# Kernel optimization log

Hardware: AMD Instinct MI355X
Metric: run time of the kernel (lower is better)

The kernel has to match this reference:

```python
import jax, jax.numpy as jnp
import numpy as np

B, S, T = 1024, 1024, 32
TAGS = ["O"] + [p + f"T{i}" for i in range(1, 16) for p in ("B-", "I-")] + ["B-T16"]
MASKED = -1.0e4


def _init_params(key):
    bound = float(np.sqrt(6.0 / T))
    k1, k2, k3 = jax.random.split(key, 3)
    start = np.array(jax.random.uniform(k1, (T,), minval=-bound, maxval=bound))
    trans = np.array(jax.random.uniform(k2, (T, T), minval=-bound, maxval=bound))
    end = np.array(jax.random.uniform(k3, (T,), minval=-bound, maxval=bound))
    # structural BIO masking, as in _initialize_parameters
    for i, src in enumerate(TAGS):
        if src.startswith("I-"):
            start[i] = MASKED
        for j, tgt in enumerate(TAGS):
            if (src.startswith("B-") or src.startswith("I-")) and tgt.startswith("I-") and src[2:] != tgt[2:]:
                trans[i, j] = MASKED
            elif src == "O" and tgt.startswith("I-"):
                trans[i, j] = MASKED
    return jnp.asarray(start, jnp.float32), jnp.asarray(trans, jnp.float32), jnp.asarray(end, jnp.float32)


def setup_inputs() -> dict:
    key = jax.random.key(0)
    k_em, k_tag, k_len, k_par = jax.random.split(key, 4)
    emissions = jax.random.normal(k_em, (B, S, T), dtype=jnp.float32)
    tags = jax.random.randint(k_tag, (B, S), 0, T, dtype=jnp.int64) if jax.config.jax_enable_x64 else jax.random.randint(k_tag, (B, S), 0, T).astype(jnp.int32)
    lengths = jax.random.randint(k_len, (B,), S // 4, S + 1)
    mask = jnp.arange(S)[None, :] < lengths[:, None]  # prefix mask, bool [B, S]
    start_transitions, transitions, end_transitions = _init_params(k_par)
    return {
        "emissions": emissions,
        "tags": tags,
        "mask": mask,
        "start_transitions": start_transitions,
        "transitions": transitions,
        "end_transitions": end_transitions,
    }


def reference(emissions, tags, mask, start_transitions, transitions, end_transitions):
    b, s, t = emissions.shape
    ar = jnp.arange(s)
    bidx = jnp.arange(b)
    head = jnp.min(jnp.where(mask, ar[None, :], s - 1), axis=1)  # [B]
    tail = jnp.max(ar[None, :] * mask, axis=1)                   # [B]
    nonempty = mask.sum(axis=1) != 0

    # condition[:, j-1] == (mask[:, j] and head != j), for j = 1..S-1
    cond = mask[:, 1:] & (head[:, None] != ar[None, 1:])  # [B, S-1]

    # ---- numerator (gold path score): additive, fully vectorized ----
    head_tags = tags[bidx, head]
    tail_tags = tags[bidx, tail]
    em_tag = jnp.take_along_axis(emissions, tags[:, :, None], axis=2)[:, :, 0]  # [B, S]
    trans_step = transitions[tags[:, :-1], tags[:, 1:]]                          # [B, S-1]
    numerator = (start_transitions[head_tags]
                 + em_tag[bidx, head]
                 + jnp.sum(jnp.where(cond, trans_step + em_tag[:, 1:], 0.0), axis=1)
                 + end_transitions[tail_tags])
    numerator = jnp.where(nonempty, numerator, 0.0)

    # ---- denominator (log partition): scan over time ----
    score0 = start_transitions[None, :] + emissions[bidx, head]  # [B, T]

    def step(score, xs):
        em_j, cond_j = xs  # [B, T], [B]
        nxt = jax.nn.logsumexp(score[:, :, None] + transitions[None, :, :] + em_j[:, None, :], axis=1)
        return jnp.where(cond_j[:, None], nxt, score), None

    em_seq = jnp.moveaxis(emissions[:, 1:, :], 1, 0)  # [S-1, B, T]
    cond_seq = jnp.moveaxis(cond, 1, 0)               # [S-1, B]
    score_final, _ = jax.lax.scan(step, score0, (em_seq, cond_seq))
    denominator = jax.nn.logsumexp(score_final + end_transitions[None, :], axis=1)
    denominator = jnp.where(nonempty, denominator, 0.0)

    # ---- token_mean reduction ----
    llh = denominator - numerator
    labels = mask.sum(axis=1).astype(emissions.dtype)
    eps = 1e-6
    return jnp.sum(llh / (labels + eps)) / (jnp.sum(labels != 0).astype(emissions.dtype) + eps)
```

## Files before the change

### kernel.cpp

```cpp
#include <hip/hip_runtime.h>
#include <cstdint>

static constexpr int S = 1024;
static constexpr int T = 32;
static constexpr float L2E  = 1.4426950408889634f;
static constexpr float LN2f = 0.6931471805599453f;

typedef __attribute__((ext_vector_type(8)))  short  short8;
typedef __attribute__((ext_vector_type(16))) float  float16;

union Frag { unsigned u[4]; short8 s; };

__global__ void crf_zero(float* ws) { ws[0] = 0.0f; ws[1] = 0.0f; }

__global__ void crf_fin(const float* __restrict__ ws, float* __restrict__ out) {
  out[0] = ws[0] / (ws[1] + 1e-6f);
}

__device__ __forceinline__ float bcast_lane(float v, int k) {
  return __uint_as_float((unsigned)__builtin_amdgcn_readlane((int)__float_as_uint(v), k));
}

__device__ __forceinline__ unsigned packbf(float hi, float lo) {
  unsigned h = __float_as_uint(hi), l = __float_as_uint(lo);
  return ((h + 0x8000u) & 0xFFFF0000u) | ((l + 0x8000u) >> 16);
}

__device__ __forceinline__ void plswap(unsigned& x, unsigned& y, bool hih) {
#if __has_builtin(__builtin_amdgcn_permlane32_swap)
  auto r = __builtin_amdgcn_permlane32_swap((int)x, (int)y, false, false);
  x = (unsigned)r[0]; y = (unsigned)r[1];
#else
  unsigned ex = (unsigned)__shfl_xor((int)x, 32, 64);
  unsigned ey = (unsigned)__shfl_xor((int)y, 32, 64);
  unsigned nx = hih ? ey : x;
  unsigned ny = hih ? y  : ex;
  x = nx; y = ny;
#endif
}

__global__ __launch_bounds__(512, 4) void crf_main(
    const float* __restrict__ em, const int* __restrict__ tags,
    const int* __restrict__ mask, const float* __restrict__ startT,
    const float* __restrict__ trans, const float* __restrict__ endT,
    float* __restrict__ ws)
{
  __shared__ __align__(16) float s_g[8][512];
  __shared__ __align__(16) float s_mats[8][1024];
  __shared__ float s_trans[1024];
  __shared__ int   s_tags[1024];
  __shared__ unsigned long long s_mb[16];
  __shared__ int   s_head, s_tail, s_cnt, s_K[8];
  __shared__ float s_num[8];

  const int tid = threadIdx.x;
  const int l   = tid & 63;
  const int wv  = tid >> 6;
  const int b   = blockIdx.x;
  const int n   = l & 31;
  const int h   = l >> 5;
  const bool hih = (h == 1);

  const float* emb   = em   + (size_t)b * S * T;
  const int*   maskb = mask + (size_t)b * S;
  const int*   tagsb = tags + (size_t)b * S;

  for (int i = tid; i < 1024; i += 512) { s_tags[i] = tagsb[i]; s_trans[i] = trans[i]; }
  {
    unsigned long long b0 = __ballot(maskb[wv * 128 + l] != 0);
    unsigned long long b1 = __ballot(maskb[wv * 128 + 64 + l] != 0);
    if (l == 0) { s_mb[2 * wv] = b0; s_mb[2 * wv + 1] = b1; }
  }

  Frag Alo, Ahi;
  #pragma unroll
  for (int p = 0; p < 4; ++p) {
    int k0 = 8 * h + 2 * p;
    Alo.u[p] = packbf(exp2f(trans[(k0 + 1)  * T + n] * L2E),
                      exp2f(trans[(k0 + 0)  * T + n] * L2E));
    Ahi.u[p] = packbf(exp2f(trans[(k0 + 17) * T + n] * L2E),
                      exp2f(trans[(k0 + 16) * T + n] * L2E));
  }
  __syncthreads();

  if (wv == 0) {
    int first = 0x7fffffff, last = -1, pc = 0;
    if (l < 16) {
      unsigned long long w = s_mb[l];
      if (w) {
        first = 64 * l + (int)__builtin_ctzll(w);
        last  = 64 * l + 63 - (int)__builtin_clzll(w);
        pc    = (int)__builtin_popcountll(w);
      }
    }
    #pragma unroll
    for (int d = 1; d < 64; d <<= 1) {
      first = min(first, __shfl_xor(first, d));
      last  = max(last,  __shfl_xor(last,  d));
      pc   += __shfl_xor(pc, d);
    }
    if (l == 0) { s_head = first; s_tail = last; s_cnt = pc; }
  }
  __syncthreads();
  const int cnt  = s_cnt;
  const int head = (cnt > 0) ? s_head : 0;
  const int tail = (cnt > 0) ? s_tail : 0;

  float* sgw = s_g[wv];
  Frag Blo, Bhi;
  #pragma unroll
  for (int p = 0; p < 4; ++p) {
    int k0 = 8 * h + 2 * p;
    Blo.u[p] = ((k0 == n)      ? 0x3F80u : 0u) | ((k0 + 1  == n) ? 0x3F800000u : 0u);
    Bhi.u[p] = ((k0 + 16 == n) ? 0x3F80u : 0u) | ((k0 + 17 == n) ? 0x3F800000u : 0u);
  }
  int   Kacc  = 0;
  float numer = 0.0f;
  const int cs = wv * 128;

#define FOLD(JJ, RSC) do {                                                   \
    const float* gr = sgw + (JJ) * T + 4 * h;                                \
    float4 ga = *(const float4*)(gr);                                        \
    float4 gb = *(const float4*)(gr + 8);                                    \
    float4 gc = *(const float4*)(gr + 16);                                   \
    float4 gd = *(const float4*)(gr + 24);                                   \
    float16 D = {0,0,0,0,0,0,0,0,0,0,0,0,0,0,0,0};                           \
    D = __builtin_amdgcn_mfma_f32_32x32x16_bf16(Alo.s, Blo.s, D, 0, 0, 0);   \
    D = __builtin_amdgcn_mfma_f32_32x32x16_bf16(Ahi.s, Bhi.s, D, 0, 0, 0);   \
    D[0]  *= ga.x; D[1]  *= ga.y; D[2]  *= ga.z; D[3]  *= ga.w;              \
    D[4]  *= gb.x; D[5]  *= gb.y; D[6]  *= gb.z; D[7]  *= gb.w;              \
    D[8]  *= gc.x; D[9]  *= gc.y; D[10] *= gc.z; D[11] *= gc.w;              \
    D[12] *= gd.x; D[13] *= gd.y; D[14] *= gd.z; D[15] *= gd.w;              \
    if (RSC) {                                                               \
      float mx = fmaxf(fmaxf(fmaxf(D[0], D[1]), fmaxf(D[2], D[3])),          \
                       fmaxf(fmaxf(D[4], D[5]), fmaxf(D[6], D[7])));         \
      mx = fmaxf(mx, fmaxf(fmaxf(fmaxf(D[8], D[9]),  fmaxf(D[10], D[11])),   \
                           fmaxf(fmaxf(D[12], D[13]), fmaxf(D[14], D[15]))));\
      mx = fmaxf(mx, __shfl_xor(mx, 1));  mx = fmaxf(mx, __shfl_xor(mx, 2)); \
      mx = fmaxf(mx, __shfl_xor(mx, 4));  mx = fmaxf(mx, __shfl_xor(mx, 8)); \
      mx = fmaxf(mx, __shfl_xor(mx, 16)); mx = fmaxf(mx, __shfl_xor(mx, 32));\
      int E = (int)((__float_as_uint(mx) >> 23) & 0xffu);                    \
      float sc = __uint_as_float((unsigned)(254 - E) << 23);                 \
      Kacc += E - 127;                                                       \
      _Pragma("unroll")                                                      \
      for (int q_ = 0; q_ < 16; ++q_) D[q_] *= sc;                           \
    }                                                                        \
    unsigned u0 = packbf(D[1],  D[0]),  u1 = packbf(D[3],  D[2]);            \
    unsigned u2 = packbf(D[5],  D[4]),  u3 = packbf(D[7],  D[6]);            \
    unsigned u4 = packbf(D[9],  D[8]),  u5 = packbf(D[11], D[10]);           \
    unsigned u6 = packbf(D[13], D[12]), u7 = packbf(D[15], D[14]);           \
    plswap(u0, u2, hih); plswap(u1, u3, hih);                                \
    plswap(u4, u6, hih); plswap(u5, u7, hih);                                \
    Blo.u[0] = u0; Blo.u[1] = u1; Blo.u[2] = u2; Blo.u[3] = u3;              \
    Bhi.u[0] = u4; Bhi.u[1] = u5; Bhi.u[2] = u6; Bhi.u[3] = u7;              \
  } while (0)

  for (int sb = 0; sb < 8; ++sb) {
    const int j0 = cs + 16 * sb;
    if (j0 > tail) break;
    unsigned eff = (unsigned)((s_mb[j0 >> 6] >> (j0 & 63)) & 0xFFFFull);
    if (j0 == 0) eff &= ~1u;
    if (head >= j0 && head < j0 + 16) eff &= ~(1u << (head - j0));
    if (eff == 0) continue;

    {
      const float4* src = (const float4*)(emb + (size_t)j0 * T);
      float4 v0 = src[l], v1 = src[l + 64];
      v0.x = exp2f(v0.x * L2E); v0.y = exp2f(v0.y * L2E);
      v0.z = exp2f(v0.z * L2E); v0.w = exp2f(v0.w * L2E);
      v1.x = exp2f(v1.x * L2E); v1.y = exp2f(v1.y * L2E);
      v1.z = exp2f(v1.z * L2E); v1.w = exp2f(v1.w * L2E);
      ((float4*)sgw)[l] = v0; ((float4*)sgw)[l + 64] = v1;
    }

    if (l < 16 && ((eff >> l) & 1u)) {
      int j  = j0 + l;
      int tg = s_tags[j], tp = s_tags[j - 1];
      numer += s_trans[tp * T + tg] + log2f(sgw[l * T + tg]) * LN2f;
    }

    if (eff == 0xFFFFu) {
      #pragma unroll
      for (int jj = 0; jj < 16; ++jj) FOLD(jj, ((jj & 7) == 7));
    } else {
      for (int jj = 0; jj < 16; ++jj)
        if ((eff >> jj) & 1u) FOLD(jj, true);
    }
  }
#undef FOLD

  #pragma unroll
  for (int p = 0; p < 4; ++p) {
    int k0 = 8 * h + 2 * p;
    s_mats[wv][(k0 + 0)  * T + n] = __uint_as_float(Blo.u[p] << 16);
    s_mats[wv][(k0 + 1)  * T + n] = __uint_as_float(Blo.u[p] & 0xFFFF0000u);
    s_mats[wv][(k0 + 16) * T + n] = __uint_as_float(Bhi.u[p] << 16);
    s_mats[wv][(k0 + 17) * T + n] = __uint_as_float(Bhi.u[p] & 0xFFFF0000u);
  }
  #pragma unroll
  for (int d = 1; d < 64; d <<= 1) numer += __shfl_xor(numer, d);
  if (l == 0) { s_num[wv] = numer; s_K[wv] = Kacc; }
  __syncthreads();

  if (wv == 0) {
    const int t = n;
    float em0 = emb[head * T + t];
    float sc0 = (startT[t] + em0) * L2E;
    float m0 = sc0;
    #pragma unroll
    for (int d = 1; d < 32; d <<= 1) m0 = fmaxf(m0, __shfl_xor(m0, d));
    float e = exp2f(sc0 - m0);
    float Mtot = m0;

    for (int c = 0; c < 8; ++c) {
      const float* row = &s_mats[c][t * T];
      float acc = 0.0f;
      #pragma unroll
      for (int q = 0; q < 32; ++q) acc = fmaf(row[q], bcast_lane(e, q), acc);
      e = acc;
      Mtot += (float)s_K[c];
      float mx = e;
      #pragma unroll
      for (int d = 1; d < 32; d <<= 1) mx = fmaxf(mx, __shfl_xor(mx, d));
      int E = (int)((__float_as_uint(mx) >> 23) & 0xffu);
      e *= __uint_as_float((unsigned)(254 - E) << 23);
      Mtot += (float)(E - 127);
    }

    float fv = e * exp2f(endT[t] * L2E);
    #pragma unroll
    for (int d = 1; d < 32; d <<= 1) fv += __shfl_xor(fv, d);
    float denom = (Mtot + log2f(fv)) * LN2f;

    if (l == 0 && cnt > 0) {
      float ntot = 0.0f;
      for (int wq = 0; wq < 8; ++wq) ntot += s_num[wq];
      int th = s_tags[head], tt = s_tags[tail];
      ntot += startT[th] + bcast_lane(em0, th) + endT[tt];
      atomicAdd(&ws[0], (denom - ntot) / ((float)cnt + 1e-6f));
      atomicAdd(&ws[1], 1.0f);
    }
  }
}

extern "C" void kernel_launch(void* const* d_in, const int* in_sizes, int n_in,
                              void* d_out, int out_size, void* d_ws, size_t ws_size,
                              hipStream_t stream) {
  const float* em     = (const float*)d_in[0];
  const int*   tags   = (const int*)d_in[1];
  const int*   mask   = (const int*)d_in[2];
  const float* startT = (const float*)d_in[3];
  const float* trans  = (const float*)d_in[4];
  const float* endT   = (const float*)d_in[5];
  float* out = (float*)d_out;
  float* ws  = (float*)d_ws;

  const int B = in_sizes[0] / (S * T);

  crf_zero<<<1, 1, 0, stream>>>(ws);
  crf_main<<<B, 512, 0, stream>>>(em, tags, mask, startT, trans, endT, ws);
  crf_fin<<<1, 1, 0, stream>>>(ws, out);
}
```

Before: 301.8 us.

## Balance CRF chunk split over active span, pack bf16 matrices, fuse finalize

Each wave now gets an equal share of the range from head+1 to tail, instead of a fixed 128-step slice that left waves idle past the sequence end. Per-chunk transfer matrices are stored as packed bf16 in padded shared memory, and tags are stored as shorts, which cuts LDS use. Launch bounds are raised to allow more resident blocks. Packing uses the hardware bf16 convert when available, and a last-block atomic counter replaces the separate finalize kernel. Unaligned mask windows need two-word bit shifts, and the bf16 convert rounding may differ slightly from the manual rounding it replaces.

```diff
diff --git a/kernel.cpp b/kernel.cpp
--- a/kernel.cpp
+++ b/kernel.cpp
@@ -11,19 +11,24 @@
 
 union Frag { unsigned u[4]; short8 s; };
 
-__global__ void crf_zero(float* ws) { ws[0] = 0.0f; ws[1] = 0.0f; }
-
-__global__ void crf_fin(const float* __restrict__ ws, float* __restrict__ out) {
-  out[0] = ws[0] / (ws[1] + 1e-6f);
+__global__ void crf_zero(float* ws) {
+  ws[0] = 0.0f; ws[1] = 0.0f; ((unsigned*)ws)[2] = 0u;
 }
 
 __device__ __forceinline__ float bcast_lane(float v, int k) {
   return __uint_as_float((unsigned)__builtin_amdgcn_readlane((int)__float_as_uint(v), k));
 }
 
-__device__ __forceinline__ unsigned packbf(float hi, float lo) {
-  unsigned h = __float_as_uint(hi), l = __float_as_uint(lo);
-  return ((h + 0x8000u) & 0xFFFF0000u) | ((l + 0x8000u) >> 16);
+__device__ __forceinline__ unsigned pk2(float lo, float hi) {
+#if __has_builtin(__builtin_amdgcn_cvt_pk_bf16_f32)
+  typedef __attribute__((ext_vector_type(2))) __bf16 bf162_t;
+  union { bf162_t v; unsigned u; } r;
+  r.v = __builtin_amdgcn_cvt_pk_bf16_f32(lo, hi);
+  return r.u;
+#else
+  unsigned h_ = __float_as_uint(hi), l_ = __float_as_uint(lo);
+  return ((h_ + 0x8000u) & 0xFFFF0000u) | ((l_ + 0x8000u) >> 16);
+#endif
 }
 
 __device__ __forceinline__ void plswap(unsigned& x, unsigned& y, bool hih) {
@@ -39,17 +44,17 @@
 #endif
 }
 
-__global__ __launch_bounds__(512, 4) void crf_main(
+__global__ __launch_bounds__(512, 8) void crf_main(
     const float* __restrict__ em, const int* __restrict__ tags,
     const int* __restrict__ mask, const float* __restrict__ startT,
     const float* __restrict__ trans, const float* __restrict__ endT,
-    float* __restrict__ ws)
+    float* __restrict__ ws, float* __restrict__ out, int B)
 {
-  __shared__ __align__(16) float s_g[8][512];
-  __shared__ __align__(16) float s_mats[8][1024];
+  __shared__ __align__(16) float    s_g[8 * 512];
+  __shared__ __align__(16) unsigned s_mats[8 * 544];
   __shared__ float s_trans[1024];
-  __shared__ int   s_tags[1024];
-  __shared__ unsigned long long s_mb[16];
+  __shared__ short s_tags[1024];
+  __shared__ unsigned long long s_mb[17];
   __shared__ int   s_head, s_tail, s_cnt, s_K[8];
   __shared__ float s_num[8];
 
@@ -65,21 +70,25 @@
   const int*   maskb = mask + (size_t)b * S;
   const int*   tagsb = tags + (size_t)b * S;
 
-  for (int i = tid; i < 1024; i += 512) { s_tags[i] = tagsb[i]; s_trans[i] = trans[i]; }
+  for (int i = tid; i < 1024; i += 512) {
+    s_tags[i]  = (short)tagsb[i];
+    s_trans[i] = trans[i];
+  }
   {
     unsigned long long b0 = __ballot(maskb[wv * 128 + l] != 0);
     unsigned long long b1 = __ballot(maskb[wv * 128 + 64 + l] != 0);
     if (l == 0) { s_mb[2 * wv] = b0; s_mb[2 * wv + 1] = b1; }
+    if (tid == 0) s_mb[16] = 0ull;
   }
 
   Frag Alo, Ahi;
   #pragma unroll
   for (int p = 0; p < 4; ++p) {
     int k0 = 8 * h + 2 * p;
-    Alo.u[p] = packbf(exp2f(trans[(k0 + 1)  * T + n] * L2E),
-                      exp2f(trans[(k0 + 0)  * T + n] * L2E));
-    Ahi.u[p] = packbf(exp2f(trans[(k0 + 17) * T + n] * L2E),
-                      exp2f(trans[(k0 + 16) * T + n] * L2E));
+    Alo.u[p] = pk2(exp2f(trans[(k0 + 0)  * T + n] * L2E),
+                   exp2f(trans[(k0 + 1)  * T + n] * L2E));
+    Ahi.u[p] = pk2(exp2f(trans[(k0 + 16) * T + n] * L2E),
+                   exp2f(trans[(k0 + 17) * T + n] * L2E));
   }
   __syncthreads();
 
@@ -106,7 +115,12 @@
   const int head = (cnt > 0) ? s_head : 0;
   const int tail = (cnt > 0) ? s_tail : 0;
 
-  float* sgw = s_g[wv];
+  const int span = tail - head;
+  const int Lc   = (span + 7) >> 3;
+  const int c0   = head + 1 + wv * Lc;
+  const int c1   = min(c0 + Lc, tail + 1);
+
+  float* sgw = s_g + wv * 512;
   Frag Blo, Bhi;
   #pragma unroll
   for (int p = 0; p < 4; ++p) {
@@ -116,7 +130,6 @@
   }
   int   Kacc  = 0;
   float numer = 0.0f;
-  const int cs = wv * 128;
 
 #define FOLD(JJ, RSC) do {                                                   \
     const float* gr = sgw + (JJ) * T + 4 * h;                                \
@@ -145,37 +158,39 @@
       _Pragma("unroll")                                                      \
       for (int q_ = 0; q_ < 16; ++q_) D[q_] *= sc;                           \
     }                                                                        \
-    unsigned u0 = packbf(D[1],  D[0]),  u1 = packbf(D[3],  D[2]);            \
-    unsigned u2 = packbf(D[5],  D[4]),  u3 = packbf(D[7],  D[6]);            \
-    unsigned u4 = packbf(D[9],  D[8]),  u5 = packbf(D[11], D[10]);           \
-    unsigned u6 = packbf(D[13], D[12]), u7 = packbf(D[15], D[14]);           \
+    unsigned u0 = pk2(D[0],  D[1]),  u1 = pk2(D[2],  D[3]);                  \
+    unsigned u2 = pk2(D[4],  D[5]),  u3 = pk2(D[6],  D[7]);                  \
+    unsigned u4 = pk2(D[8],  D[9]),  u5 = pk2(D[10], D[11]);                 \
+    unsigned u6 = pk2(D[12], D[13]), u7 = pk2(D[14], D[15]);                 \
     plswap(u0, u2, hih); plswap(u1, u3, hih);                                \
     plswap(u4, u6, hih); plswap(u5, u7, hih);                                \
     Blo.u[0] = u0; Blo.u[1] = u1; Blo.u[2] = u2; Blo.u[3] = u3;              \
     Bhi.u[0] = u4; Bhi.u[1] = u5; Bhi.u[2] = u6; Bhi.u[3] = u7;              \
   } while (0)
 
-  for (int sb = 0; sb < 8; ++sb) {
-    const int j0 = cs + 16 * sb;
-    if (j0 > tail) break;
-    unsigned eff = (unsigned)((s_mb[j0 >> 6] >> (j0 & 63)) & 0xFFFFull);
-    if (j0 == 0) eff &= ~1u;
-    if (head >= j0 && head < j0 + 16) eff &= ~(1u << (head - j0));
-    if (eff == 0) continue;
+  for (int j0 = c0; j0 < c1; j0 += 16) {
+    const int ns = min(16, c1 - j0);
+    const int w = j0 >> 6, o = j0 & 63;
+    unsigned long long bits = s_mb[w] >> o;
+    if (o) bits |= s_mb[w + 1] << (64 - o);
+    unsigned eff = (unsigned)(bits & 0xFFFFull) & (unsigned)((1u << ns) - 1u);
 
     {
-      const float4* src = (const float4*)(emb + (size_t)j0 * T);
-      float4 v0 = src[l], v1 = src[l + 64];
+      const int i0 = l, i1 = l + 64;
+      const int r0 = min(j0 + (i0 >> 3), S - 1), q0 = i0 & 7;
+      const int r1 = min(j0 + (i1 >> 3), S - 1), q1 = i1 & 7;
+      float4 v0 = ((const float4*)(emb + (size_t)r0 * T))[q0];
+      float4 v1 = ((const float4*)(emb + (size_t)r1 * T))[q1];
       v0.x = exp2f(v0.x * L2E); v0.y = exp2f(v0.y * L2E);
       v0.z = exp2f(v0.z * L2E); v0.w = exp2f(v0.w * L2E);
       v1.x = exp2f(v1.x * L2E); v1.y = exp2f(v1.y * L2E);
       v1.z = exp2f(v1.z * L2E); v1.w = exp2f(v1.w * L2E);
-      ((float4*)sgw)[l] = v0; ((float4*)sgw)[l + 64] = v1;
-    }
-
-    if (l < 16 && ((eff >> l) & 1u)) {
+      ((float4*)sgw)[i0] = v0; ((float4*)sgw)[i1] = v1;
+    }
+
+    if (l < ns && ((eff >> l) & 1u)) {
       int j  = j0 + l;
-      int tg = s_tags[j], tp = s_tags[j - 1];
+      int tg = (int)s_tags[j], tp = (int)s_tags[j - 1];
       numer += s_trans[tp * T + tg] + log2f(sgw[l * T + tg]) * LN2f;
     }
 
@@ -183,19 +198,19 @@
       #pragma unroll
       for (int jj = 0; jj < 16; ++jj) FOLD(jj, ((jj & 7) == 7));
     } else {
-      for (int jj = 0; jj < 16; ++jj)
+      for (int jj = 0; jj < ns; ++jj)
         if ((eff >> jj) & 1u) FOLD(jj, true);
     }
   }
 #undef FOLD
 
-  #pragma unroll
-  for (int p = 0; p < 4; ++p) {
-    int k0 = 8 * h + 2 * p;
-    s_mats[wv][(k0 + 0)  * T + n] = __uint_as_float(Blo.u[p] << 16);
-    s_mats[wv][(k0 + 1)  * T + n] = __uint_as_float(Blo.u[p] & 0xFFFF0000u);
-    s_mats[wv][(k0 + 16) * T + n] = __uint_as_float(Bhi.u[p] << 16);
-    s_mats[wv][(k0 + 17) * T + n] = __uint_as_float(Bhi.u[p] & 0xFFFF0000u);
+  {
+    unsigned* mw = s_mats + wv * 544;
+    #pragma unroll
+    for (int p = 0; p < 4; ++p) {
+      mw[(4 * h + p)     * 34 + n] = Blo.u[p];
+      mw[(4 * h + p + 8) * 34 + n] = Bhi.u[p];
+    }
   }
   #pragma unroll
   for (int d = 1; d < 64; d <<= 1) numer += __shfl_xor(numer, d);
@@ -204,7 +219,7 @@
 
   if (wv == 0) {
     const int t = n;
-    float em0 = emb[head * T + t];
+    const float em0 = emb[head * T + t];
     float sc0 = (startT[t] + em0) * L2E;
     float m0 = sc0;
     #pragma unroll
@@ -212,11 +227,18 @@
     float e = exp2f(sc0 - m0);
     float Mtot = m0;
 
+    const unsigned sh = (t & 1) ? 0u : 16u;
     for (int c = 0; c < 8; ++c) {
-      const float* row = &s_mats[c][t * T];
+      const unsigned* mw = s_mats + c * 544 + (t >> 1) * 34;
       float acc = 0.0f;
       #pragma unroll
-      for (int q = 0; q < 32; ++q) acc = fmaf(row[q], bcast_lane(e, q), acc);
+      for (int q2 = 0; q2 < 16; ++q2) {
+        uint2 w2 = *(const uint2*)(mw + 2 * q2);
+        float vlo = __uint_as_float((w2.x << sh) & 0xFFFF0000u);
+        float vhi = __uint_as_float((w2.y << sh) & 0xFFFF0000u);
+        acc = fmaf(vlo, bcast_lane(e, 2 * q2), acc);
+        acc = fmaf(vhi, bcast_lane(e, 2 * q2 + 1), acc);
+      }
       e = acc;
       Mtot += (float)s_K[c];
       float mx = e;
@@ -232,13 +254,21 @@
     for (int d = 1; d < 32; d <<= 1) fv += __shfl_xor(fv, d);
     float denom = (Mtot + log2f(fv)) * LN2f;
 
-    if (l == 0 && cnt > 0) {
-      float ntot = 0.0f;
-      for (int wq = 0; wq < 8; ++wq) ntot += s_num[wq];
-      int th = s_tags[head], tt = s_tags[tail];
-      ntot += startT[th] + bcast_lane(em0, th) + endT[tt];
-      atomicAdd(&ws[0], (denom - ntot) / ((float)cnt + 1e-6f));
-      atomicAdd(&ws[1], 1.0f);
+    if (l == 0) {
+      if (cnt > 0) {
+        float ntot = 0.0f;
+        for (int wq = 0; wq < 8; ++wq) ntot += s_num[wq];
+        int th = (int)s_tags[head], tt = (int)s_tags[tail];
+        ntot += startT[th] + bcast_lane(em0, th) + endT[tt];
+        atomicAdd(&ws[0], (denom - ntot) / ((float)cnt + 1e-6f));
+        atomicAdd(&ws[1], 1.0f);
+      }
+      __threadfence();
+      unsigned done = atomicAdd((unsigned*)ws + 2, 1u);
+      if (done == (unsigned)(B - 1)) {
+        __threadfence();
+        out[0] = ws[0] / (ws[1] + 1e-6f);
+      }
     }
   }
 }
@@ -258,6 +288,5 @@
   const int B = in_sizes[0] / (S * T);
 
   crf_zero<<<1, 1, 0, stream>>>(ws);
-  crf_main<<<B, 512, 0, stream>>>(em, tags, mask, startT, trans, endT, ws);
-  crf_fin<<<1, 1, 0, stream>>>(ws, out);
-}
+  crf_main<<<B, 512, 0, stream>>>(em, tags, mask, startT, trans, endT, ws, out, B);
+}
```

After: 302.6 us. No clear change (+0.3%).
